# Optimization experiments

Hardware: AMD Instinct MI355X
Metric: run time of the kernel (lower is better)

Reference implementation:

```python
import jax, jax.numpy as jnp
import numpy as np

B, T, U = 4, 300, 60
ENC_D, DEC_D = 512, 512
INPUT_DIM, INNER_DIM, VOCAB = 1024, 1024, 1000


def setup_inputs() -> dict:
    key = jax.random.key(0)
    ks = jax.random.split(key, 6)
    return {
        "enc_state": jax.random.normal(ks[0], (B, T, ENC_D), dtype=jnp.float32),
        "dec_state": jax.random.normal(ks[1], (B, U, DEC_D), dtype=jnp.float32),
        "W1": jax.random.normal(ks[2], (INPUT_DIM, INNER_DIM), dtype=jnp.float32) * (1.0 / np.sqrt(INPUT_DIM)),
        "b1": jax.random.normal(ks[3], (INNER_DIM,), dtype=jnp.float32) * 0.01,
        "W2": jax.random.normal(ks[4], (INNER_DIM, VOCAB), dtype=jnp.float32) * (1.0 / np.sqrt(INNER_DIM)),
        "b2": jax.random.normal(ks[5], (VOCAB,), dtype=jnp.float32) * 0.01,
    }


def reference(enc_state, dec_state, W1, b1, W2, b2):
    # Original: broadcast enc to (B,T,U,enc_d), dec to (B,T,U,dec_d), concat -> Linear -> tanh -> Linear.
    # Equivalent (same math, no huge concat): split W1 into enc/dec blocks and add broadcasted projections.
    W1_enc, W1_dec = W1[:ENC_D], W1[ENC_D:]
    enc_proj = jnp.einsum('btd,dh->bth', enc_state, W1_enc)  # (B,T,H)
    dec_proj = jnp.einsum('bud,dh->buh', dec_state, W1_dec)  # (B,U,H)
    hidden = jnp.tanh(enc_proj[:, :, None, :] + dec_proj[:, None, :, :] + b1)  # (B,T,U,H)
    logits = jnp.einsum('btuh,hv->btuv', hidden, W2) + b2  # (B,T,U,V)
    return logits
```

## Files before the change

kernel.cpp:

```cpp
#include <hip/hip_runtime.h>
#include <hip/hip_bf16.h>
#include <stdint.h>

#define B_  4
#define T_  300
#define U_  60
#define V_  1000
#define M_TOT (B_*T_*U_)
#define MBCNT 282
#define WK  1056
#define PK  1040

typedef __attribute__((ext_vector_type(8))) short short8;
typedef __attribute__((ext_vector_type(4))) float f32x4;
typedef __attribute__((ext_vector_type(4))) int int4v;

__device__ __forceinline__ short f2bf(float f) {
    union { float f; uint32_t u; } c; c.f = f;
    uint32_t u = c.u;
    uint32_t r = (u + 0x7FFFu + ((u >> 16) & 1u)) >> 16;
    return (short)r;
}

__device__ __forceinline__ float fast_tanh(float x) {
    float e = __expf(2.0f * x);
    float r = __builtin_amdgcn_rcpf(e + 1.0f);
    return 1.0f - 2.0f * r;
}

__device__ __forceinline__ void gl_lds16(const void* g, void* l) {
    __builtin_amdgcn_global_load_lds(
        (const __attribute__((address_space(1))) void*)g,
        (__attribute__((address_space(3))) void*)l, 16, 0, 0);
}


__global__ void transpose_cvt(const float* __restrict__ in, short* __restrict__ out,
                              int R, int C, int ostride) {
    __shared__ float tile[64][65];
    const int tx = threadIdx.x & 63, ty = threadIdx.x >> 6;
    const int r0 = blockIdx.y * 64, c0 = blockIdx.x * 64;
#pragma unroll
    for (int i = 0; i < 16; ++i) {
        int r = r0 + i * 4 + ty, c = c0 + tx;
        float v = 0.f;
        if (r < R && c < C) v = in[(long)r * C + c];
        tile[i * 4 + ty][tx] = v;
    }
    __syncthreads();
#pragma unroll
    for (int i = 0; i < 16; ++i) {
        int oc = c0 + i * 4 + ty;
        int orr = r0 + tx;
        out[(long)oc * ostride + orr] = f2bf(tile[tx][i * 4 + ty]);
    }
}

__global__ void transpose_pack_w2(const float* __restrict__ in, short* __restrict__ out) {
    __shared__ float tile[64][65];
    const int tx = threadIdx.x & 63, ty = threadIdx.x >> 6;
    const int r0 = blockIdx.y * 64, c0 = blockIdx.x * 64;
#pragma unroll
    for (int i = 0; i < 16; ++i) {
        int r = r0 + i * 4 + ty, c = c0 + tx;
        float v = 0.f;
        if (c < V_) v = in[(long)r * V_ + c];
        tile[i * 4 + ty][tx] = v;
    }
    __syncthreads();
#pragma unroll
    for (int i = 0; i < 16; ++i) {
        int oc = c0 + i * 4 + ty;
        int orr = r0 + tx;
        int nb = oc >> 8, pr = oc & 255, h = pr >> 7, rr = pr & 127;
        int t = orr >> 6, kk = orr & 63;
        out[(long)((nb * 16 + t) * 2 + h) * 8192 + rr * 64 + kk] =
            f2bf(tile[tx][i * 4 + ty]);
    }
}

__global__ __launch_bounds__(256, 2) void proj_gemm(
        const float* __restrict__ X, int M, int k_off,
        const short* __restrict__ Wt,
        const float* __restrict__ b1,
        float* __restrict__ P)
{
    __shared__ short As[64 * 64];
    const int tid = threadIdx.x;
    const int lane = tid & 63;
    const int w = tid >> 6;
    const int wm = w >> 1, wn = w & 1;
    const int m0 = blockIdx.x * 64, n0 = blockIdx.y * 64;

    f32x4 acc[2][2] = {};
    for (int k0 = 0; k0 < 512; k0 += 64) {
#pragma unroll
        for (int c = 0; c < 2; ++c) {
            int lin = tid + 256 * c;
            int row = lin >> 3, k8 = lin & 7;
            int m = m0 + row;
            short vals[8];
            if (m < M) {
                const float* xp = X + (long)m * 512 + k0 + k8 * 8;
#pragma unroll
                for (int j = 0; j < 8; ++j) vals[j] = f2bf(xp[j]);
            } else {
#pragma unroll
                for (int j = 0; j < 8; ++j) vals[j] = 0;
            }
            int byte = row * 128 + k8 * 16;
            byte ^= (row & 7) << 4;
            *(int4v*)((char*)As + byte) = *(const int4v*)vals;
        }
        __syncthreads();
#pragma unroll
        for (int ks = 0; ks < 2; ++ks) {
            short8 af[2];
#pragma unroll
            for (int mf = 0; mf < 2; ++mf) {
                int row = wm * 32 + mf * 16 + (lane & 15);
                int byte = row * 128 + ks * 64 + (lane >> 4) * 16;
                byte ^= (row & 7) << 4;
                af[mf] = *(const short8*)((char*)As + byte);
            }
#pragma unroll
            for (int nf = 0; nf < 2; ++nf) {
                int h = n0 + wn * 32 + nf * 16 + (lane & 15);
                const short* bp = Wt + (long)h * WK + k_off + k0 + ks * 32 + (lane >> 4) * 8;
                short8 bfv = *(const short8*)bp;
#pragma unroll
                for (int mf = 0; mf < 2; ++mf)
                    acc[mf][nf] = __builtin_amdgcn_mfma_f32_16x16x32_bf16(af[mf], bfv, acc[mf][nf], 0, 0, 0);
            }
        }
        __syncthreads();
    }
#pragma unroll
    for (int mf = 0; mf < 2; ++mf)
#pragma unroll
        for (int nf = 0; nf < 2; ++nf) {
            int h = n0 + wn * 32 + nf * 16 + (lane & 15);
            float bb = b1 ? b1[h] : 0.f;
#pragma unroll
            for (int j = 0; j < 4; ++j) {
                int m = m0 + wm * 32 + mf * 16 + (lane >> 4) * 4 + j;
                if (m < M) P[(long)m * PK + h] = acc[mf][nf][j] + bb;
            }
        }
}

__global__ __launch_bounds__(256) void hgen_pk(
        const float* __restrict__ encP, const float* __restrict__ decP,
        short* __restrict__ Hp)
{
    long idx = (long)blockIdx.x * 256 + threadIdx.x;
    int u = (int)(idx >> 10);
    int gi = (int)(idx & 1023);
    int mb = u >> 5, rem = u & 31, t = rem >> 1, h = rem & 1;
    int r = gi >> 3, kg = gi & 7;
    int m = mb * 256 + h * 128 + r;
    int k = t * 64 + kg * 8;
    short8 v = {};
    if (m < M_TOT) {
        int bt = m / U_;
        int uu = m - bt * U_;
        int b = m / (T_ * U_);
        const float* e = encP + (long)bt * PK + k;
        const float* d = decP + (long)(b * U_ + uu) * PK + k;
        f32x4 e0 = *(const f32x4*)(e), e1 = *(const f32x4*)(e + 4);
        f32x4 d0 = *(const f32x4*)(d), d1 = *(const f32x4*)(d + 4);
#pragma unroll
        for (int j = 0; j < 4; ++j) v[j]     = f2bf(fast_tanh(e0[j] + d0[j]));
#pragma unroll
        for (int j = 0; j < 4; ++j) v[4 + j] = f2bf(fast_tanh(e1[j] + d1[j]));
    }
    *(short8*)(Hp + (long)u * 8192 + gi * 8) = v;
}

__global__ __launch_bounds__(512, 2) void gemm8p(
        const short* __restrict__ Hp,
        const short* __restrict__ W2p,
        const float* __restrict__ b2,
        float* __restrict__ out)
{
    __shared__ __align__(16) char lds[131072];

    const int tid = threadIdx.x;
    const int lane = tid & 63;
    const int w = tid >> 6;
    const int wm = w >> 2, wn = w & 3;
    const int l15 = lane & 15, ksel = lane >> 4;

    const int nwg = gridDim.x;
    int bid = blockIdx.x;
    int q = nwg >> 3, r = nwg & 7;
    int xcd = bid & 7, lq = bid >> 3;
    int wg = (xcd < r ? xcd * (q + 1) : r * (q + 1) + (xcd - r) * q) + lq;
    const int mb = wg >> 2, nb = wg & 3;

    const int rowA = tid >> 3;
    const int gA = (tid & 7) ^ (rowA & 7);
    const short* aSrc = Hp  + (long)mb * 262144 + rowA * 64 + gA * 8;
    const short* bSrc = W2p + (long)nb * 262144 + rowA * 64 + gA * 8;
    const int wq = w << 10;

#define ST_A(uidx_, roff_) do {                                              \
    gl_lds16(aSrc + (long)(uidx_) * 8192, (char*)lds + (roff_) + wq);        \
    gl_lds16(aSrc + (long)(uidx_) * 8192 + 4096,                             \
             (char*)lds + (roff_) + 8192 + wq);                              \
} while (0)
#define ST_B(uidx_, roff_) do {                                              \
    gl_lds16(bSrc + (long)(uidx_) * 8192, (char*)lds + (roff_) + wq);        \
    gl_lds16(bSrc + (long)(uidx_) * 8192 + 4096,                             \
             (char*)lds + (roff_) + 8192 + wq);                              \
} while (0)

    short8 af[4][2], bf0[2][2], bf1[2][2];
    f32x4 acc[8][4] = {};

#define RD_AF(d_, qm_) do {                                                  \
    _Pragma("unroll")                                                        \
    for (int mf = 0; mf < 4; ++mf) {                                         \
        const int rw_ = wm * 64 + mf * 16 + l15;                             \
        const char* bp_ = (const char*)lds + (d_) * 65536 + (qm_) * 16384    \
                          + rw_ * 128;                                       \
        const int sx_ = (rw_ & 7) << 4;                                      \
        af[mf][0] = *(const short8*)(bp_ + ((ksel * 16) ^ sx_));             \
        af[mf][1] = *(const short8*)(bp_ + ((64 + ksel * 16) ^ sx_));        \
    } } while (0)

#define RD_BF(d_, qn_, B_) do {                                              \
    _Pragma("unroll")                                                        \
    for (int nf = 0; nf < 2; ++nf) {                                         \
        const int rw_ = wn * 32 + nf * 16 + l15;                             \
        const char* bp_ = (const char*)lds + (d_) * 65536 + 32768            \
                          + (qn_) * 16384 + rw_ * 128;                       \
        const int sx_ = (rw_ & 7) << 4;                                      \
        B_[nf][0] = *(const short8*)(bp_ + ((ksel * 16) ^ sx_));             \
        B_[nf][1] = *(const short8*)(bp_ + ((64 + ksel * 16) ^ sx_));        \
    } } while (0)

#define MM(qm_, qn_, B_) do {                                                \
    __builtin_amdgcn_s_setprio(1);                                           \
    _Pragma("unroll")                                                        \
    for (int kh = 0; kh < 2; ++kh)                                           \
        _Pragma("unroll")                                                    \
        for (int nf = 0; nf < 2; ++nf)                                       \
            _Pragma("unroll")                                                \
            for (int mf = 0; mf < 4; ++mf)                                   \
                acc[(qm_) * 4 + mf][(qn_) * 2 + nf] =                        \
                    __builtin_amdgcn_mfma_f32_16x16x32_bf16(                 \
                        af[mf][kh], B_[nf][kh],                              \
                        acc[(qm_) * 4 + mf][(qn_) * 2 + nf], 0, 0, 0);       \
    __builtin_amdgcn_s_setprio(0);                                           \
} while (0)

#define GATE(n_) asm volatile("s_waitcnt vmcnt(" #n_ ")" ::: "memory")
#define BARC do {                                                            \
    __builtin_amdgcn_s_barrier();                                            \
    asm volatile("s_waitcnt lgkmcnt(0)" ::: "memory");                       \
    __builtin_amdgcn_sched_barrier(0);                                       \
} while (0)
#define BARE __builtin_amdgcn_s_barrier()

#define TILE(t_, c_, n_, G3_) do {                                           \
                                                     \
    RD_AF(c_, 0); RD_BF(c_, 0, bf0);                                         \
    ST_B(((t_) + 1) * 2,     (n_) * 65536 + 32768);                          \
    GATE(6);                                                                 \
    asm volatile("s_waitcnt lgkmcnt(8)" ::: "memory");                       \
    BARC; MM(0, 0, bf0); BARE;                                               \
                                                              \
    RD_BF(c_, 1, bf1);                                                       \
    ST_B(((t_) + 1) * 2 + 1, (n_) * 65536 + 49152);                          \
    GATE(6);                                                                 \
    BARC; MM(0, 1, bf1); BARE;                                               \
                                                              \
    RD_AF(c_, 1);                                                            \
    ST_A(((t_) + 1) * 2 + 1, (n_) * 65536 + 16384);                          \
    BARC; MM(1, 0, bf0); BARE;                                               \
                                                              \
    ST_A(((t_) + 2) * 2,     (c_) * 65536);                                  \
    G3_;                                                                     \
    BARC; MM(1, 1, bf1); BARE;                                               \
} while (0)

    ST_A(0, 0);
    ST_B(0, 32768);
    ST_B(1, 49152);
    ST_A(1, 16384);
    ST_A(2, 65536);
    GATE(6);
    BARE;

#pragma unroll 1
    for (int tt = 0; tt < 14; tt += 2) {
        TILE(tt,     0, 1, GATE(6));
        TILE(tt + 1, 1, 0, GATE(6));
    }
    RD_AF(0, 0); RD_BF(0, 0, bf0);
    ST_B(30, 65536 + 32768);
    GATE(6);
    asm volatile("s_waitcnt lgkmcnt(8)" ::: "memory");
    BARC; MM(0, 0, bf0); BARE;
    RD_BF(0, 1, bf1);
    ST_B(31, 65536 + 49152);
    GATE(6);
    BARC; MM(0, 1, bf1); BARE;
    RD_AF(0, 1);
    ST_A(31, 65536 + 16384);
    BARC; MM(1, 0, bf0); BARE;
    GATE(4);
    BARC; MM(1, 1, bf1); BARE;
    RD_AF(1, 0); RD_BF(1, 0, bf0);
    GATE(2);
    BARC; MM(0, 0, bf0); BARE;
    RD_BF(1, 1, bf1);
    GATE(0);
    BARC; MM(0, 1, bf1); BARE;
    RD_AF(1, 1);
    BARC; MM(1, 0, bf0); BARE;
    BARC; MM(1, 1, bf1);

#pragma unroll
    for (int qn = 0; qn < 2; ++qn)
#pragma unroll
        for (int nf = 0; nf < 2; ++nf) {
            int n = nb * 256 + qn * 128 + wn * 32 + nf * 16 + l15;
            if (n < V_) {
                float bv = b2[n];
#pragma unroll
                for (int qm = 0; qm < 2; ++qm)
#pragma unroll
                    for (int mf = 0; mf < 4; ++mf)
#pragma unroll
                        for (int j = 0; j < 4; ++j) {
                            int m = mb * 256 + qm * 128 + wm * 64 + mf * 16 + ksel * 4 + j;
                            if (m < M_TOT)
                                out[(long)m * V_ + n] = acc[qm * 4 + mf][qn * 2 + nf][j] + bv;
                        }
            }
        }
#undef ST_A
#undef ST_B
#undef RD_AF
#undef RD_BF
#undef MM
#undef GATE
#undef BARC
#undef BARE
#undef TILE
}

__global__ __launch_bounds__(512, 2) void joint_gemm(
        const float* __restrict__ encP, const float* __restrict__ decP,
        const short* __restrict__ W2t, const float* __restrict__ b2,
        float* __restrict__ out)
{
    __shared__ short As[2][64 * 64];
    const int tid = threadIdx.x;
    const int lane = tid & 63;
    const int w = tid >> 6;
    const int m0 = blockIdx.x * 64;
    const int n0 = blockIdx.y * 512;

    const int arow = tid >> 3;
    const int k8 = tid & 7;
    const int am = m0 + arow;
    const int bt = am / U_;
    const int u = am - bt * U_;
    const int bidx = am / (T_ * U_);
    const float* eptr = encP + (long)bt * PK + k8 * 8;
    const float* dptr = decP + (long)(bidx * U_ + u) * PK + k8 * 8;
    const int wbyte = (arow * 128 + k8 * 16) ^ ((arow & 7) << 4);

    f32x4 acc[4][4] = {};
    const short* bbase[4];
#pragma unroll
    for (int nf = 0; nf < 4; ++nf) {
        int n = n0 + w * 64 + nf * 16 + (lane & 15);
        bbase[nf] = W2t + (long)n * WK + (lane >> 4) * 8;
    }
    f32x4 e0 = *(const f32x4*)(eptr), e1 = *(const f32x4*)(eptr + 4);
    f32x4 d0 = *(const f32x4*)(dptr), d1 = *(const f32x4*)(dptr + 4);
    {
        short vals[8];
#pragma unroll
        for (int j = 0; j < 4; ++j) vals[j]     = f2bf(fast_tanh(e0[j] + d0[j]));
#pragma unroll
        for (int j = 0; j < 4; ++j) vals[4 + j] = f2bf(fast_tanh(e1[j] + d1[j]));
        *(int4v*)((char*)&As[0][0] + wbyte) = *(const int4v*)vals;
    }
    e0 = *(const f32x4*)(eptr + 64); e1 = *(const f32x4*)(eptr + 68);
    d0 = *(const f32x4*)(dptr + 64); d1 = *(const f32x4*)(dptr + 68);
    asm volatile("s_waitcnt lgkmcnt(0)" ::: "memory");
    __builtin_amdgcn_s_barrier();

#pragma unroll 1
    for (int t = 0; t < 16; ++t) {
        const int k0 = t * 64;
        short8 bfr[2][4];
#pragma unroll
        for (int ks = 0; ks < 2; ++ks)
#pragma unroll
            for (int nf = 0; nf < 4; ++nf)
                bfr[ks][nf] = *(const short8*)(bbase[nf] + k0 + ks * 32);
        if (t < 15) {
            short vals[8];
#pragma unroll
            for (int j = 0; j < 4; ++j) vals[j]     = f2bf(fast_tanh(e0[j] + d0[j]));
#pragma unroll
            for (int j = 0; j < 4; ++j) vals[4 + j] = f2bf(fast_tanh(e1[j] + d1[j]));
            *(int4v*)((char*)&As[(t & 1) ^ 1][0] + wbyte) = *(const int4v*)vals;
            if (t < 14) {
                e0 = *(const f32x4*)(eptr + k0 + 128); e1 = *(const f32x4*)(eptr + k0 + 132);
                d0 = *(const f32x4*)(dptr + k0 + 128); d1 = *(const f32x4*)(dptr + k0 + 132);
            }
        }
        const char* rb = (const char*)&As[t & 1][0];
#pragma unroll
        for (int ks = 0; ks < 2; ++ks) {
            short8 af[4];
#pragma unroll
            for (int mf = 0; mf < 4; ++mf) {
                int row = mf * 16 + (lane & 15);
                int byte = (row * 128 + ks * 64 + (lane >> 4) * 16) ^ ((row & 7) << 4);
                af[mf] = *(const short8*)(rb + byte);
            }
#pragma unroll
            for (int nf = 0; nf < 4; ++nf)
#pragma unroll
                for (int mf = 0; mf < 4; ++mf)
                    acc[mf][nf] = __builtin_amdgcn_mfma_f32_16x16x32_bf16(
                        af[mf], bfr[ks][nf], acc[mf][nf], 0, 0, 0);
        }
        if (t < 15) {
            asm volatile("s_waitcnt lgkmcnt(0)" ::: "memory");
            __builtin_amdgcn_s_barrier();
        }
    }
#pragma unroll
    for (int nf = 0; nf < 4; ++nf) {
        int n = n0 + w * 64 + nf * 16 + (lane & 15);
        float bv = (n < V_) ? b2[n] : 0.f;
#pragma unroll
        for (int mf = 0; mf < 4; ++mf)
#pragma unroll
            for (int j = 0; j < 4; ++j) {
                int m = m0 + mf * 16 + (lane >> 4) * 4 + j;
                if (n < V_)
                    out[(long)m * V_ + n] = acc[mf][nf][j] + bv;
            }
    }
}

extern "C" void kernel_launch(void* const* d_in, const int* in_sizes, int n_in,
                              void* d_out, int out_size, void* d_ws, size_t ws_size,
                              hipStream_t stream) {
    const float* enc = (const float*)d_in[0];
    const float* dec = (const float*)d_in[1];
    const float* W1  = (const float*)d_in[2];
    const float* b1  = (const float*)d_in[3];
    const float* W2  = (const float*)d_in[4];
    const float* b2  = (const float*)d_in[5];
    float* out = (float*)d_out;

    char* ws = (char*)d_ws;
    size_t off = 0;
    short* W1t  = (short*)(ws + off); off += (size_t)1024 * WK * 2;
    short* W2p  = (short*)(ws + off); off += (size_t)1024 * WK * 2;
    float* encP = (float*)(ws + off); off += (size_t)1200 * PK * 4;
    float* decP = (float*)(ws + off); off += (size_t)240 * PK * 4;
    short* Hp   = (short*)(ws + off);
    size_t need = off + (size_t)MBCNT * 262144 * 2;

    transpose_cvt<<<dim3(16, 16), 256, 0, stream>>>(W1, W1t, 1024, 1024, WK);
    proj_gemm<<<dim3(19, 16), 256, 0, stream>>>(enc, 1200, 0,   W1t, nullptr, encP);
    proj_gemm<<<dim3(4, 16),  256, 0, stream>>>(dec, 240,  512, W1t, b1,      decP);

    if (ws_size >= need) {
        transpose_pack_w2<<<dim3(16, 16), 256, 0, stream>>>(W2, W2p);
        hgen_pk<<<MBCNT * 32 * 1024 / 256, 256, 0, stream>>>(encP, decP, Hp);
        gemm8p<<<MBCNT * 4, 512, 0, stream>>>(Hp, W2p, b2, out);
    } else {
        short* W2t = W2p;
        transpose_cvt<<<dim3(16, 16), 256, 0, stream>>>(W2, W2t, 1024, 1000, WK);
        joint_gemm<<<dim3(1125, 2), 512, 0, stream>>>(encP, decP, W2t, b2, out);
    }
}
```

Before: 339.7 us.

## Replace 8-phase GEMM pipeline with simpler 2-phase double-buffered K loop

Restructures the main bf16 MFMA GEMM's K-loop from an eight-barrier-per-tile interleaved schedule (quarter-tile loads and MMA chunks) to a two-phase scheme. Each iteration issues all global-to-LDS stores for the next tile, waits, then does the full tile's MMAs with two barriers. This aims to cut barrier and synchronisation overhead, at the cost of coarser overlap between global loads and compute. Waiting on vmcnt(8) also changes how many loads are in flight.

```diff
diff --git a/kernel.cpp b/kernel.cpp
--- a/kernel.cpp
+++ b/kernel.cpp
@@ -177,7 +177,7 @@
     *(short8*)(Hp + (long)u * 8192 + gi * 8) = v;
 }
 
-__global__ __launch_bounds__(512, 2) void gemm8p(
+__global__ __launch_bounds__(512, 2) void gemm2p(
         const short* __restrict__ Hp,
         const short* __restrict__ W2p,
         const float* __restrict__ b2,
@@ -240,87 +240,65 @@
         B_[nf][1] = *(const short8*)(bp_ + ((64 + ksel * 16) ^ sx_));        \
     } } while (0)
 
-#define MM(qm_, qn_, B_) do {                                                \
+#define MMQ(qm_) do {                                                        \
     __builtin_amdgcn_s_setprio(1);                                           \
     _Pragma("unroll")                                                        \
-    for (int kh = 0; kh < 2; ++kh)                                           \
+    for (int kh = 0; kh < 2; ++kh) {                                         \
         _Pragma("unroll")                                                    \
         for (int nf = 0; nf < 2; ++nf)                                       \
             _Pragma("unroll")                                                \
             for (int mf = 0; mf < 4; ++mf)                                   \
-                acc[(qm_) * 4 + mf][(qn_) * 2 + nf] =                        \
+                acc[(qm_) * 4 + mf][nf] =                                    \
                     __builtin_amdgcn_mfma_f32_16x16x32_bf16(                 \
-                        af[mf][kh], B_[nf][kh],                              \
-                        acc[(qm_) * 4 + mf][(qn_) * 2 + nf], 0, 0, 0);       \
+                        af[mf][kh], bf0[nf][kh], acc[(qm_) * 4 + mf][nf], 0, 0, 0); \
+        _Pragma("unroll")                                                    \
+        for (int nf = 0; nf < 2; ++nf)                                       \
+            _Pragma("unroll")                                                \
+            for (int mf = 0; mf < 4; ++mf)                                   \
+                acc[(qm_) * 4 + mf][2 + nf] =                                \
+                    __builtin_amdgcn_mfma_f32_16x16x32_bf16(                 \
+                        af[mf][kh], bf1[nf][kh], acc[(qm_) * 4 + mf][2 + nf], 0, 0, 0); \
+    }                                                                        \
     __builtin_amdgcn_s_setprio(0);                                           \
 } while (0)
 
-#define GATE(n_) asm volatile("s_waitcnt vmcnt(" #n_ ")" ::: "memory")
-#define BARC do {                                                            \
-    __builtin_amdgcn_s_barrier();                                            \
+#define LGKM0 do {                                                           \
     asm volatile("s_waitcnt lgkmcnt(0)" ::: "memory");                       \
     __builtin_amdgcn_sched_barrier(0);                                       \
 } while (0)
-#define BARE __builtin_amdgcn_s_barrier()
-
-#define TILE(t_, c_, n_, G3_) do {                                           \
-                                                     \
-    RD_AF(c_, 0); RD_BF(c_, 0, bf0);                                         \
-    ST_B(((t_) + 1) * 2,     (n_) * 65536 + 32768);                          \
-    GATE(6);                                                                 \
-    asm volatile("s_waitcnt lgkmcnt(8)" ::: "memory");                       \
-    BARC; MM(0, 0, bf0); BARE;                                               \
-                                                              \
-    RD_BF(c_, 1, bf1);                                                       \
-    ST_B(((t_) + 1) * 2 + 1, (n_) * 65536 + 49152);                          \
-    GATE(6);                                                                 \
-    BARC; MM(0, 1, bf1); BARE;                                               \
-                                                              \
-    RD_AF(c_, 1);                                                            \
-    ST_A(((t_) + 1) * 2 + 1, (n_) * 65536 + 16384);                          \
-    BARC; MM(1, 0, bf0); BARE;                                               \
-                                                              \
-    ST_A(((t_) + 2) * 2,     (c_) * 65536);                                  \
-    G3_;                                                                     \
-    BARC; MM(1, 1, bf1); BARE;                                               \
+
+#define TILE2(t_, cur_, nxt_, GATE_) do {                                    \
+    if ((t_) < 15) {                                                         \
+        ST_A(((t_) + 1) * 2,     (nxt_) * 65536);                            \
+        ST_A(((t_) + 1) * 2 + 1, (nxt_) * 65536 + 16384);                    \
+        ST_B(((t_) + 1) * 2,     (nxt_) * 65536 + 32768);                    \
+        ST_B(((t_) + 1) * 2 + 1, (nxt_) * 65536 + 49152);                    \
+    }                                                                        \
+    asm volatile("s_waitcnt vmcnt(" GATE_ ")" ::: "memory");                 \
+    __builtin_amdgcn_s_barrier();                                            \
+    __builtin_amdgcn_sched_barrier(0);                                       \
+    RD_AF(cur_, 0); RD_BF(cur_, 0, bf0); RD_BF(cur_, 1, bf1);                \
+    LGKM0;                                                                   \
+    MMQ(0);                                                                  \
+    RD_AF(cur_, 1);                                                          \
+    LGKM0;                                                                   \
+    MMQ(1);                                                                  \
+    __builtin_amdgcn_s_barrier();                                            \
 } while (0)
 
     ST_A(0, 0);
+    ST_A(1, 16384);
     ST_B(0, 32768);
     ST_B(1, 49152);
-    ST_A(1, 16384);
-    ST_A(2, 65536);
-    GATE(6);
-    BARE;
+    asm volatile("s_waitcnt vmcnt(0)" ::: "memory");
+    __builtin_amdgcn_s_barrier();
 
 #pragma unroll 1
-    for (int tt = 0; tt < 14; tt += 2) {
-        TILE(tt,     0, 1, GATE(6));
-        TILE(tt + 1, 1, 0, GATE(6));
-    }
-    RD_AF(0, 0); RD_BF(0, 0, bf0);
-    ST_B(30, 65536 + 32768);
-    GATE(6);
-    asm volatile("s_waitcnt lgkmcnt(8)" ::: "memory");
-    BARC; MM(0, 0, bf0); BARE;
-    RD_BF(0, 1, bf1);
-    ST_B(31, 65536 + 49152);
-    GATE(6);
-    BARC; MM(0, 1, bf1); BARE;
-    RD_AF(0, 1);
-    ST_A(31, 65536 + 16384);
-    BARC; MM(1, 0, bf0); BARE;
-    GATE(4);
-    BARC; MM(1, 1, bf1); BARE;
-    RD_AF(1, 0); RD_BF(1, 0, bf0);
-    GATE(2);
-    BARC; MM(0, 0, bf0); BARE;
-    RD_BF(1, 1, bf1);
-    GATE(0);
-    BARC; MM(0, 1, bf1); BARE;
-    RD_AF(1, 1);
-    BARC; MM(1, 0, bf0); BARE;
-    BARC; MM(1, 1, bf1);
+    for (int t = 0; t < 15; ++t) {
+        const int cur = t & 1;
+        TILE2(t, cur, cur ^ 1, "8");
+    }
+    TILE2(15, 1, 0, "0");
 
 #pragma unroll
     for (int qn = 0; qn < 2; ++qn)
@@ -345,11 +323,9 @@
 #undef ST_B
 #undef RD_AF
 #undef RD_BF
-#undef MM
-#undef GATE
-#undef BARC
-#undef BARE
-#undef TILE
+#undef MMQ
+#undef LGKM0
+#undef TILE2
 }
 
 __global__ __launch_bounds__(512, 2) void joint_gemm(
@@ -481,7 +457,7 @@
     if (ws_size >= need) {
         transpose_pack_w2<<<dim3(16, 16), 256, 0, stream>>>(W2, W2p);
         hgen_pk<<<MBCNT * 32 * 1024 / 256, 256, 0, stream>>>(encP, decP, Hp);
-        gemm8p<<<MBCNT * 4, 512, 0, stream>>>(Hp, W2p, b2, out);
+        gemm2p<<<MBCNT * 4, 512, 0, stream>>>(Hp, W2p, b2, out);
     } else {
         short* W2t = W2p;
         transpose_cvt<<<dim3(16, 16), 256, 0, stream>>>(W2, W2t, 1024, 1000, WK);
```

Measured after the change: 364.6 us. +7.3%, slower.
